# Kernel optimization log

Hardware: AMD Instinct MI355X
Metric: run time of the kernel (lower is better)

Reference implementation:

```python
import jax, jax.numpy as jnp
import numpy as np

IN_FEATURES = 1024
N_CLASSES = 50257
CUTOFFS = [2000, 10000]      # head covers [0,2000); clusters [2000,10000), [10000,50257)
DIV_VALUE = 4.0
IGNORE_INDEX = -1
N_ROWS = 4096
HEAD_SIZE = CUTOFFS[0] + len(CUTOFFS)  # 2002 (head classes + one slot per tail cluster)
HSZ = [int(IN_FEATURES // (DIV_VALUE ** (i + 1))) for i in range(len(CUTOFFS))]  # [256, 64]
BOUNDS = CUTOFFS + [N_CLASSES]


def setup_inputs() -> dict:
    key = jax.random.key(0)
    ks = jax.random.split(key, 8)
    x = jax.random.normal(ks[0], (N_ROWS, IN_FEATURES), dtype=jnp.float32)
    target = jax.random.randint(ks[1], (N_ROWS,), 0, N_CLASSES, dtype=jnp.int64)
    drop = jax.random.uniform(ks[2], (N_ROWS,)) < 0.1
    target = jnp.where(drop, IGNORE_INDEX, target)
    s = 1.0 / np.sqrt(IN_FEATURES)
    head_w = jax.random.normal(ks[3], (HEAD_SIZE, IN_FEATURES), dtype=jnp.float32) * s
    proj0 = jax.random.normal(ks[4], (HSZ[0], IN_FEATURES), dtype=jnp.float32) * s
    out0 = jax.random.normal(ks[5], (BOUNDS[1] - BOUNDS[0], HSZ[0]), dtype=jnp.float32) * (1.0 / np.sqrt(HSZ[0]))
    proj1 = jax.random.normal(ks[6], (HSZ[1], IN_FEATURES), dtype=jnp.float32) * s
    out1 = jax.random.normal(ks[7], (BOUNDS[2] - BOUNDS[1], HSZ[1]), dtype=jnp.float32) * (1.0 / np.sqrt(HSZ[1]))
    return {"x": x, "target": target, "head_w": head_w,
            "proj0": proj0, "out0": out0, "proj1": proj1, "out1": out1}


def reference(x, target, head_w, proj0, out0, proj1, out1):
    # head: [N, cutoff0 + n_clusters] logits, shared log-softmax
    head_lp = jax.nn.log_softmax(jnp.einsum('nd,hd->nh', x, head_w), axis=-1)
    rows = jnp.arange(x.shape[0])
    valid = target != IGNORE_INDEX
    t = jnp.where(valid, target, 0)

    # head-band targets: log prob directly from head
    t_head = jnp.clip(t, 0, CUTOFFS[0] - 1)
    logp = head_lp[rows, t_head]

    # tail clusters: head cluster-slot logprob + within-cluster logprob
    tails = [(proj0, out0), (proj1, out1)]
    for i, (proj, out) in enumerate(tails):
        low, high = BOUNDS[i], BOUNDS[i + 1]
        # [N, hsz] @ [hsz, osz] -> [N, osz] cluster logits
        cl_lp = jax.nn.log_softmax(
            jnp.einsum('nh,oh->no', jnp.einsum('nd,hd->nh', x, proj), out), axis=-1)
        rel = jnp.clip(t - low, 0, high - low - 1)
        cand = head_lp[:, CUTOFFS[0] + i] + cl_lp[rows, rel]
        logp = jnp.where((t >= low) & (t < high), cand, logp)

    # ignore-index filter + mean == masked mean over valid rows
    vf = valid.astype(logp.dtype)
    loss = -(logp * vf).sum() / vf.sum()
    return loss
```

## Files before the change

### kernel.cpp

```cpp
#include <hip/hip_runtime.h>
#include <hip/hip_bf16.h>

typedef __attribute__((ext_vector_type(8))) short bf16x8;
typedef __attribute__((ext_vector_type(4))) float f32x4;
typedef unsigned short u16;

constexpr int NR      = 4096;
constexpr int INF     = 1024;
constexpr int HEAD_N  = 2002;
constexpr int HEAD_NP = 2048;
constexpr int C0_LO   = 2000, C0_HI = 10000;
constexpr int C0_N    = 8000;
constexpr int C1_N    = 40257;
constexpr int C1_NP   = 40320;
constexpr int K0      = 256;
constexpr int K1      = 64;
constexpr int PCAT    = 320;
constexpr int PCAT_P  = 384;
constexpr int WCAT_R  = HEAD_NP + PCAT_P;
constexpr int IGNORE  = -1;
constexpr float LOG2E = 1.4426950408889634f;
constexpr float LN2   = 0.6931471805599453f;

constexpr int S0      = 50;
constexpr int TPS0    = 5;
constexpr int S1      = 40;
constexpr int TPS1    = 8;
constexpr int NHP     = 32;
constexpr int HEADB   = 512;
constexpr int C1B     = 32 * S1;
constexpr int C0B     = 32 * S0;
constexpr int MEGA_GRID = HEADB + C1B + C0B;

static __device__ __forceinline__ u16 f32_to_bf16(float f) {
    unsigned int u = __float_as_uint(f);
    return (u16)((u + 0x7FFFu + ((u >> 16) & 1u)) >> 16);
}
static __device__ __forceinline__ float bf2f(u16 v) {
    unsigned int u = ((unsigned int)v) << 16;
    return __uint_as_float(u);
}

static __device__ __forceinline__ float fast_exp2(float x) {
#if __has_builtin(__builtin_amdgcn_exp2f)
    return __builtin_amdgcn_exp2f(x);
#else
    return __expf(x * LN2);
#endif
}

static __device__ __forceinline__ void gload_lds16(const u16* g, u16* l) {
    __builtin_amdgcn_global_load_lds(
        (const __attribute__((address_space(1))) unsigned int*)g,
        (__attribute__((address_space(3))) unsigned int*)l, 16, 0, 0);
}

struct CvtSegs { const float* s[6]; u16* d[6]; int n8[6]; float sc[6]; };

__global__ void cvt_compact(CvtSegs segs, const int* __restrict__ tgt,
                            int* __restrict__ c0list, int* __restrict__ c1list,
                            int* __restrict__ crow, int* __restrict__ cnts) {
    if (blockIdx.x == 0) {
        __shared__ int b0s, b1s;
        const int tid = threadIdx.x;
        const int lane = tid & 63;
        if (tid == 0) { b0s = 0; b1s = 0; }
        __syncthreads();
        for (int it = 0; it < NR / 256; ++it) {
            const int r = it * 256 + tid;
            const int t = tgt[r];
            const bool in0 = (t >= C0_LO) && (t < C0_HI);
            const bool in1 = (t >= C0_HI);
            unsigned long long m0 = __ballot(in0);
            unsigned long long m1 = __ballot(in1);
            int base0 = 0, base1 = 0;
            if (lane == 0) {
                base0 = atomicAdd(&b0s, (int)__popcll(m0));
                base1 = atomicAdd(&b1s, (int)__popcll(m1));
            }
            base0 = __shfl(base0, 0, 64);
            base1 = __shfl(base1, 0, 64);
            const unsigned long long lt = (1ULL << lane) - 1ULL;
            if (in0) { int s = base0 + (int)__popcll(m0 & lt); c0list[s] = r; crow[r] = s; }
            else if (in1) { int s = base1 + (int)__popcll(m1 & lt); c1list[s] = r; crow[r] = s; }
            else crow[r] = 0;
        }
        __syncthreads();
        const int c0 = b0s, c1 = b1s;
        const int p0 = (c0 + 127) & ~127, p1 = (c1 + 127) & ~127;
        if (threadIdx.x == 0) { cnts[0] = c0; cnts[1] = c1; cnts[2] = p0; cnts[3] = p1; }
        for (int i = c0 + (int)threadIdx.x; i < p0; i += 256) c0list[i] = 0;
        for (int i = c1 + (int)threadIdx.x; i < p1; i += 256) c1list[i] = 0;
    }

    const int stride = gridDim.x * blockDim.x;
    const int gid = blockIdx.x * blockDim.x + threadIdx.x;
#pragma unroll
    for (int seg = 0; seg < 6; ++seg) {
        const float4* sp = (const float4*)segs.s[seg];
        bf16x8* dp = (bf16x8*)segs.d[seg];
        const int n8 = segs.n8[seg];
        const float sc = segs.sc[seg];
        for (int i = gid; i < n8; i += stride) {
            float4 a = sp[2 * i], b = sp[2 * i + 1];
            bf16x8 o;
            o[0] = (short)f32_to_bf16(a.x * sc); o[1] = (short)f32_to_bf16(a.y * sc);
            o[2] = (short)f32_to_bf16(a.z * sc); o[3] = (short)f32_to_bf16(a.w * sc);
            o[4] = (short)f32_to_bf16(b.x * sc); o[5] = (short)f32_to_bf16(b.y * sc);
            o[6] = (short)f32_to_bf16(b.z * sc); o[7] = (short)f32_to_bf16(b.w * sc);
            dp[i] = o;
        }
    }
}

__launch_bounds__(256, 2)
__global__ void proj_tile(const u16* __restrict__ A, const u16* __restrict__ B,
                          u16* __restrict__ HB)
{
    constexpr int K = INF;
    __shared__ u16 ldsA[128 * 64];
    __shared__ u16 ldsB[128 * 64];
    const int tid = threadIdx.x, wid = tid >> 6, lane = tid & 63;
    const int wr = wid >> 1, wc = wid & 1;
    const int row0 = blockIdx.x * 128, col0 = blockIdx.y * 128;

    f32x4 acc[4][4];
#pragma unroll
    for (int m = 0; m < 4; ++m)
#pragma unroll
        for (int n = 0; n < 4; ++n) acc[m][n] = (f32x4){0.f, 0.f, 0.f, 0.f};

    const int srow = lane >> 3;
    const int ssw  = (lane & 7) ^ srow;

    for (int ks = 0; ks < K / 64; ++ks) {
        const int k0 = ks * 64;
#pragma unroll
        for (int q = 0; q < 4; ++q) {
            const int c = q * 4 + wid, row = c * 8 + srow;
            gload_lds16(A + (size_t)(row0 + row) * K + k0 + ssw * 8, ldsA + c * 512);
        }
#pragma unroll
        for (int q = 0; q < 4; ++q) {
            const int c = q * 4 + wid, row = c * 8 + srow;
            gload_lds16(B + (size_t)(col0 + row) * K + k0 + ssw * 8, ldsB + c * 512);
        }
        __syncthreads();
        const bf16x8* A8 = (const bf16x8*)ldsA;
        const bf16x8* B8 = (const bf16x8*)ldsB;
        bf16x8 af[4][2], bfr[4][2];
#pragma unroll
        for (int m = 0; m < 4; ++m) {
            const int ar = wr * 64 + m * 16 + (lane & 15);
#pragma unroll
            for (int ks2 = 0; ks2 < 2; ++ks2)
                af[m][ks2] = A8[ar * 8 + ((ks2 * 4 + (lane >> 4)) ^ (ar & 7))];
        }
#pragma unroll
        for (int n = 0; n < 4; ++n) {
            const int br = wc * 64 + n * 16 + (lane & 15);
#pragma unroll
            for (int ks2 = 0; ks2 < 2; ++ks2)
                bfr[n][ks2] = B8[br * 8 + ((ks2 * 4 + (lane >> 4)) ^ (br & 7))];
        }
#pragma unroll
        for (int ks2 = 0; ks2 < 2; ++ks2)
#pragma unroll
            for (int m = 0; m < 4; ++m)
#pragma unroll
                for (int n = 0; n < 4; ++n)
                    acc[m][n] = __builtin_amdgcn_mfma_f32_16x16x32_bf16(
                        af[m][ks2], bfr[n][ks2], acc[m][n], 0, 0, 0);
        __syncthreads();
    }
#pragma unroll
    for (int m = 0; m < 4; ++m)
#pragma unroll
        for (int n = 0; n < 4; ++n) {
            const int col = col0 + wc * 64 + n * 16 + (lane & 15);
            if (col < PCAT) {
#pragma unroll
                for (int r = 0; r < 4; ++r) {
                    const int row = row0 + wr * 64 + m * 16 + (lane >> 4) * 4 + r;
                    HB[(size_t)row * PCAT + col] = f32_to_bf16(acc[m][n][r]);
                }
            }
        }
}

static __device__ void head_section(int rb, int ct,
                                    const u16* __restrict__ A, const u16* __restrict__ B,
                                    const int* __restrict__ tgt,
                                    float* __restrict__ SEHp, float* __restrict__ TL,
                                    u16* ldsA, u16* ldsB, int* sth)
{
    constexpr int K = INF;
    const int tid = threadIdx.x, wid = tid >> 6, lane = tid & 63;
    const int wr = wid >> 1, wc = wid & 1;
    const int row0 = rb * 128, col0 = ct * 128;

    if (tid < 128) {
        int t = tgt[row0 + tid];
        sth[tid] = (t < 0) ? 0 : (t < C0_LO ? t : (t < C0_HI ? C0_LO : C0_LO + 1));
    }

    f32x4 acc[4][4];
#pragma unroll
    for (int m = 0; m < 4; ++m)
#pragma unroll
        for (int n = 0; n < 4; ++n) acc[m][n] = (f32x4){0.f, 0.f, 0.f, 0.f};

    const int srow = lane >> 3;
    const int ssw  = (lane & 7) ^ srow;

    for (int ks = 0; ks < K / 64; ++ks) {
        const int k0 = ks * 64;
#pragma unroll
        for (int q = 0; q < 4; ++q) {
            const int c = q * 4 + wid, row = c * 8 + srow;
            gload_lds16(A + (size_t)(row0 + row) * K + k0 + ssw * 8, ldsA + c * 512);
        }
#pragma unroll
        for (int q = 0; q < 4; ++q) {
            const int c = q * 4 + wid, row = c * 8 + srow;
            gload_lds16(B + (size_t)(col0 + row) * K + k0 + ssw * 8, ldsB + c * 512);
        }
        __syncthreads();
        const bf16x8* A8 = (const bf16x8*)ldsA;
        const bf16x8* B8 = (const bf16x8*)ldsB;
        bf16x8 af[4][2], bfr[4][2];
#pragma unroll
        for (int m = 0; m < 4; ++m) {
            const int ar = wr * 64 + m * 16 + (lane & 15);
#pragma unroll
            for (int ks2 = 0; ks2 < 2; ++ks2)
                af[m][ks2] = A8[ar * 8 + ((ks2 * 4 + (lane >> 4)) ^ (ar & 7))];
        }
#pragma unroll
        for (int n = 0; n < 4; ++n) {
            const int br = wc * 64 + n * 16 + (lane & 15);
#pragma unroll
            for (int ks2 = 0; ks2 < 2; ++ks2)
                bfr[n][ks2] = B8[br * 8 + ((ks2 * 4 + (lane >> 4)) ^ (br & 7))];
        }
#pragma unroll
        for (int ks2 = 0; ks2 < 2; ++ks2)
#pragma unroll
            for (int m = 0; m < 4; ++m)
#pragma unroll
                for (int n = 0; n < 4; ++n)
                    acc[m][n] = __builtin_amdgcn_mfma_f32_16x16x32_bf16(
                        af[m][ks2], bfr[n][ks2], acc[m][n], 0, 0, 0);
        __syncthreads();
    }

    const int slot = ct * 2 + wc;
#pragma unroll
    for (int m = 0; m < 4; ++m) {
        f32x4 rs = (f32x4){0.f, 0.f, 0.f, 0.f};
#pragma unroll
        for (int n = 0; n < 4; ++n) {
            const int cls = col0 + wc * 64 + n * 16 + (lane & 15);
            if (cls < HEAD_N) {
#pragma unroll
                for (int r = 0; r < 4; ++r) {
                    rs[r] += fast_exp2(acc[m][n][r]);
                    const int lrow = wr * 64 + m * 16 + (lane >> 4) * 4 + r;
                    if (sth[lrow] == cls) TL[row0 + lrow] = acc[m][n][r];
                }
            }
        }
#pragma unroll
        for (int msk = 1; msk < 16; msk <<= 1)
#pragma unroll
            for (int r = 0; r < 4; ++r) rs[r] += __shfl_xor(rs[r], msk, 64);
        if ((lane & 15) == 0) {
            const int rbase = row0 + wr * 64 + m * 16 + (lane >> 4) * 4;
#pragma unroll
            for (int r = 0; r < 4; ++r) SEHp[(size_t)slot * NR + rbase + r] = rs[r];
        }
    }
}

template<int K, int CT>
static __device__ void sumexp_section(const u16* __restrict__ Hbase, int ldh,
                                      const int* __restrict__ list,
                                      const u16* __restrict__ W,
                                      int nreal, int ntiles, int tps,
                                      int rb, int split, float* __restrict__ SEp,
                                      u16* lds)
{
    constexpr int MSETS = 2;
    constexpr int NKF   = K / 32;
    constexpr int SLOTS = K / 8;
    constexpr int CHUNKS = CT * K * 2 / 4096;
    constexpr int RPC   = 256 / SLOTS;
    constexpr int NT    = CT / 16;

    const int tid = threadIdx.x, wid = tid >> 6, lane = tid & 63;
    const int row0 = rb * 128 + wid * 32;

    const int t0 = split * tps;
    const int t1 = min(t0 + tps, ntiles);

    bf16x8 afr[MSETS][NKF];
#pragma unroll
    for (int m = 0; m < MSETS; ++m) {
        const int orow = list[row0 + m * 16 + (lane & 15)];
        const u16* hr = Hbase + (size_t)orow * ldh + (lane >> 4) * 8;
#pragma unroll
        for (int kf = 0; kf < NKF; ++kf)
            afr[m][kf] = *(const bf16x8*)(hr + kf * 32);
    }

    float rs[MSETS][4];
#pragma unroll
    for (int m = 0; m < MSETS; ++m)
#pragma unroll
        for (int r = 0; r < 4; ++r) rs[m][r] = 0.f;

    const int trow  = tid / SLOTS;
    const int swoff = ((tid % SLOTS) ^ (trow & 7)) * 8;

    auto STAGE = [&](int t, int buf) {
        const u16* wb = W + (size_t)t * CT * K + (size_t)trow * K + swoff;
        u16* lb = lds + buf * (CT * K) + wid * 512;
#pragma unroll
        for (int c = 0; c < CHUNKS; ++c)
            gload_lds16(wb + (size_t)c * RPC * K, lb + c * 2048);
    };

    int cur = 0;
    STAGE(t0, 0);
    __syncthreads();

    for (int t = t0; t < t1; ++t) {
        if (t + 1 < t1) STAGE(t + 1, cur ^ 1);
        const bf16x8* B8 = (const bf16x8*)(lds + cur * (CT * K));
        const bool full = (t + 1) * CT <= nreal;
#pragma unroll
        for (int n = 0; n < NT; ++n) {
            const int br = n * 16 + (lane & 15);
            bf16x8 bfr[NKF];
#pragma unroll
            for (int kf = 0; kf < NKF; ++kf)
                bfr[kf] = B8[br * SLOTS + ((kf * 4 + (lane >> 4)) ^ (br & 7))];
            f32x4 acc[MSETS];
#pragma unroll
            for (int m = 0; m < MSETS; ++m) acc[m] = (f32x4){0.f, 0.f, 0.f, 0.f};
#pragma unroll
            for (int m = 0; m < MSETS; ++m)
#pragma unroll
                for (int kf = 0; kf < NKF; ++kf)
                    acc[m] = __builtin_amdgcn_mfma_f32_16x16x32_bf16(
                        afr[m][kf], bfr[kf], acc[m], 0, 0, 0);
            if (full || (t * CT + n * 16 + (lane & 15)) < nreal) {
#pragma unroll
                for (int m = 0; m < MSETS; ++m)
#pragma unroll
                    for (int r = 0; r < 4; ++r) rs[m][r] += fast_exp2(acc[m][r]);
            }
        }
        __syncthreads();
        cur ^= 1;
    }

#pragma unroll
    for (int msk = 1; msk < 16; msk <<= 1)
#pragma unroll
        for (int m = 0; m < MSETS; ++m)
#pragma unroll
            for (int r = 0; r < 4; ++r) rs[m][r] += __shfl_xor(rs[m][r], msk, 64);
    if ((lane & 15) == 0) {
        const int rbase = row0 + (lane >> 4) * 4;
#pragma unroll
        for (int m = 0; m < MSETS; ++m)
#pragma unroll
            for (int r = 0; r < 4; ++r)
                SEp[(size_t)split * NR + rbase + m * 16 + r] = rs[m][r];
    }
}

__launch_bounds__(256, 4)
__global__ void mega_kernel(const u16* __restrict__ xb, const u16* __restrict__ wcatb,
                            const u16* __restrict__ hcatb,
                            const u16* __restrict__ o0b, const u16* __restrict__ o1b,
                            const int* __restrict__ tgt,
                            const int* __restrict__ c0list, const int* __restrict__ c1list,
                            const int* __restrict__ cnts,
                            float* __restrict__ SEHp, float* __restrict__ TL,
                            float* __restrict__ C0p, float* __restrict__ C1p)
{
    __shared__ u16 smem[2][8192];
    __shared__ int sth[128];
    const int bid = blockIdx.x;

    if (bid < HEADB) {
        head_section(bid >> 4, bid & 15, xb, wcatb, tgt, SEHp, TL,
                     smem[0], smem[1], sth);
    } else if (bid < HEADB + C1B) {
        const int c = bid - HEADB;
        const int rb = c / S1, split = c - rb * S1;
        if (rb * 128 < cnts[3])
            sumexp_section<K1, 128>(hcatb + 256, PCAT, c1list, o1b,
                                    C1_N, C1_NP / 128, TPS1, rb, split, C1p, smem[0]);
    } else {
        const int idx = bid - (HEADB + C1B);
        const int rb = idx / S0, split = idx - rb * S0;
        if (rb * 128 < cnts[2])
            sumexp_section<K0, 32>(hcatb, PCAT, c0list, o0b,
                                   C0_N, C0_N / 32, TPS0, rb, split, C0p, smem[0]);
    }
}

__global__ void epilogue_kernel(const int* __restrict__ tgt, const float* __restrict__ tl,
                                const float* __restrict__ out0, const float* __restrict__ out1,
                                const u16* __restrict__ hcatb,
                                const float* __restrict__ SEHp, const float* __restrict__ C0p,
                                const float* __restrict__ C1p, const int* __restrict__ crow,
                                float* __restrict__ rowlogp, float* __restrict__ rowvalid) {
    const int wid = threadIdx.x >> 6, lane = threadIdx.x & 63;
    const int r = blockIdx.x * 4 + wid;
    const int t = tgt[r];
    const bool valid = (t != IGNORE);
    const int tc = valid ? t : 0;
    const int band = (tc < C0_LO) ? 0 : (tc < C0_HI) ? 1 : 2;
    const int cr = crow[r];

    float p2 = 0.f;
    if (band == 1) {
        const u16* hr = hcatb + (size_t)r * PCAT;
        const float* crp = out0 + (size_t)(tc - C0_LO) * K0;
        for (int k = lane; k < K0; k += 64) p2 += bf2f(hr[k]) * crp[k];
    } else if (band == 2) {
        p2 = bf2f(hcatb[(size_t)r * PCAT + 256 + lane]) * out1[(size_t)(tc - C0_HI) * K1 + lane];
    }
#pragma unroll
    for (int msk = 32; msk >= 1; msk >>= 1) p2 += __shfl_xor(p2, msk, 64);

    float hp = (lane < NHP) ? SEHp[(size_t)lane * NR + r] : 0.f;
    float cp = 0.f;
    if (band == 1 && lane < S0) cp = C0p[(size_t)lane * NR + cr];
    if (band == 2 && lane < S1) cp = C1p[(size_t)lane * NR + cr];
#pragma unroll
    for (int msk = 1; msk < 64; msk <<= 1) {
        hp += __shfl_xor(hp, msk, 64);
        cp += __shfl_xor(cp, msk, 64);
    }

    if (lane == 0) {
        float logp = LN2 * tl[r] - __logf(hp);
        if (band != 0) logp += p2 - __logf(cp);
        rowlogp[r]  = valid ? logp : 0.f;
        rowvalid[r] = valid ? 1.f : 0.f;
    }
}

__global__ void final_reduce(const float* __restrict__ rowlogp,
                             const float* __restrict__ rowvalid, float* __restrict__ out) {
    __shared__ float sl[256], sv[256];
    const int tid = threadIdx.x;
    float a = 0.f, b = 0.f;
    for (int i = tid; i < NR; i += 256) { a += rowlogp[i]; b += rowvalid[i]; }
    sl[tid] = a; sv[tid] = b;
    __syncthreads();
    for (int s = 128; s > 0; s >>= 1) {
        if (tid < s) { sl[tid] += sl[tid + s]; sv[tid] += sv[tid + s]; }
        __syncthreads();
    }
    if (tid == 0) out[0] = -sl[0] / sv[0];
}

extern "C" void kernel_launch(void* const* d_in, const int* in_sizes, int n_in,
                              void* d_out, int out_size, void* d_ws, size_t ws_size,
                              hipStream_t stream) {
    const float* x      = (const float*)d_in[0];
    const int*   tgt    = (const int*)d_in[1];
    const float* head_w = (const float*)d_in[2];
    const float* proj0  = (const float*)d_in[3];
    const float* out0   = (const float*)d_in[4];
    const float* proj1  = (const float*)d_in[5];
    const float* out1   = (const float*)d_in[6];
    float* loss = (float*)d_out;

    char* base = (char*)d_ws;
    size_t off = 0;
    auto alloc = [&](size_t bytes) { char* p = base + off; off += (bytes + 255) & ~(size_t)255; return p; };

    u16* xb    = (u16*)alloc((size_t)NR * INF * 2);
    u16* wcatb = (u16*)alloc((size_t)WCAT_R * INF * 2);
    u16* o0b   = (u16*)alloc((size_t)C0_N * K0 * 2);
    u16* o1b   = (u16*)alloc((size_t)C1_NP * K1 * 2);
    u16* hcatb = (u16*)alloc((size_t)NR * PCAT * 2);
    float* SEHp = (float*)alloc((size_t)NHP * NR * 4);
    float* C0p  = (float*)alloc((size_t)S0 * NR * 4);
    float* C1p  = (float*)alloc((size_t)S1 * NR * 4);
    float* tl   = (float*)alloc((size_t)NR * 4);
    int* c0list = (int*)alloc((size_t)(NR + 128) * 4);
    int* c1list = (int*)alloc((size_t)(NR + 128) * 4);
    int* crow   = (int*)alloc((size_t)NR * 4);
    int* cnts   = (int*)alloc(4 * 4);
    float* rowlogp  = (float*)alloc((size_t)NR * 4);
    float* rowvalid = (float*)alloc((size_t)NR * 4);

    CvtSegs segs;
    segs.s[0] = x;      segs.d[0] = xb;                              segs.n8[0] = NR * INF / 8;      segs.sc[0] = 1.0f;
    segs.s[1] = head_w; segs.d[1] = wcatb;                           segs.n8[1] = HEAD_N * INF / 8;  segs.sc[1] = LOG2E;
    segs.s[2] = proj0;  segs.d[2] = wcatb + (size_t)HEAD_NP * INF;   segs.n8[2] = 256 * INF / 8;     segs.sc[2] = 1.0f;
    segs.s[3] = proj1;  segs.d[3] = wcatb + (size_t)(HEAD_NP + 256) * INF; segs.n8[3] = 64 * INF / 8; segs.sc[3] = 1.0f;
    segs.s[4] = out0;   segs.d[4] = o0b;                             segs.n8[4] = C0_N * K0 / 8;     segs.sc[4] = LOG2E;
    segs.s[5] = out1;   segs.d[5] = o1b;                             segs.n8[5] = C1_N * K1 / 8;     segs.sc[5] = LOG2E;
    cvt_compact<<<2048, 256, 0, stream>>>(segs, tgt, c0list, c1list, crow, cnts);

    proj_tile<<<dim3(32, PCAT_P / 128), 256, 0, stream>>>(xb, wcatb + (size_t)HEAD_NP * INF, hcatb);

    mega_kernel<<<MEGA_GRID, 256, 0, stream>>>(xb, wcatb, hcatb, o0b, o1b, tgt,
                                               c0list, c1list, cnts, SEHp, tl, C0p, C1p);

    epilogue_kernel<<<NR / 4, 256, 0, stream>>>(tgt, tl, out0, out1, hcatb,
                                                SEHp, C0p, C1p, crow, rowlogp, rowvalid);
    final_reduce<<<1, 256, 0, stream>>>(rowlogp, rowvalid, loss);
    (void)in_sizes; (void)n_in; (void)out_size; (void)ws_size;
}
```

Before: 88.86 us.

## Fuse projection GEMM into conversion kernel and interleave mega-kernel work with grid-stride loops

Removes the separate proj_tile launch by computing the x·[proj0;proj1] projection inside the conversion kernel. Dedicated blocks read fp32 x and proj weights directly, convert them to bf16 in registers and run MFMA without LDS staging, while the remaining blocks convert x, head_w, out0 and out1. The mega-kernel now interleaves head, cluster-1 and cluster-0 work across block IDs and uses grid-stride loops bounded by the actual compacted counts, so fewer blocks exit idle. In exchange, the fused projection reloads proj rows from global memory per warp without tiling reuse, which may be slow and sits on the critical path of the conversion kernel.

```diff
diff --git a/kernel.cpp b/kernel.cpp
--- a/kernel.cpp
+++ b/kernel.cpp
@@ -16,8 +16,6 @@
 constexpr int K0      = 256;
 constexpr int K1      = 64;
 constexpr int PCAT    = 320;
-constexpr int PCAT_P  = 384;
-constexpr int WCAT_R  = HEAD_NP + PCAT_P;
 constexpr int IGNORE  = -1;
 constexpr float LOG2E = 1.4426950408889634f;
 constexpr float LN2   = 0.6931471805599453f;
@@ -27,10 +25,9 @@
 constexpr int S1      = 40;
 constexpr int TPS1    = 8;
 constexpr int NHP     = 32;
-constexpr int HEADB   = 512;
-constexpr int C1B     = 32 * S1;
-constexpr int C0B     = 32 * S0;
-constexpr int MEGA_GRID = HEADB + C1B + C0B;
+constexpr int NPROJB  = 128;
+constexpr int CVT_GRID = 2048;
+constexpr int MEGA_GRID = 1792;
 
 static __device__ __forceinline__ u16 f32_to_bf16(float f) {
     unsigned int u = __float_as_uint(f);
@@ -39,6 +36,14 @@
 static __device__ __forceinline__ float bf2f(u16 v) {
     unsigned int u = ((unsigned int)v) << 16;
     return __uint_as_float(u);
+}
+static __device__ __forceinline__ bf16x8 cvt8(float4 a, float4 b, float sc) {
+    bf16x8 o;
+    o[0] = (short)f32_to_bf16(a.x * sc); o[1] = (short)f32_to_bf16(a.y * sc);
+    o[2] = (short)f32_to_bf16(a.z * sc); o[3] = (short)f32_to_bf16(a.w * sc);
+    o[4] = (short)f32_to_bf16(b.x * sc); o[5] = (short)f32_to_bf16(b.y * sc);
+    o[6] = (short)f32_to_bf16(b.z * sc); o[7] = (short)f32_to_bf16(b.w * sc);
+    return o;
 }
 
 static __device__ __forceinline__ float fast_exp2(float x) {
@@ -55,15 +60,53 @@
         (__attribute__((address_space(3))) unsigned int*)l, 16, 0, 0);
 }
 
-struct CvtSegs { const float* s[6]; u16* d[6]; int n8[6]; float sc[6]; };
-
-__global__ void cvt_compact(CvtSegs segs, const int* __restrict__ tgt,
-                            int* __restrict__ c0list, int* __restrict__ c1list,
-                            int* __restrict__ crow, int* __restrict__ cnts) {
-    if (blockIdx.x == 0) {
+struct CvtSegs { const float* s[4]; u16* d[4]; int n8[4]; float sc[4]; };
+
+__global__ void cvtproj_kernel(CvtSegs segs,
+                               const float* __restrict__ x,
+                               const float* __restrict__ proj0, const float* __restrict__ proj1,
+                               u16* __restrict__ hcatb,
+                               const int* __restrict__ tgt,
+                               int* __restrict__ c0list, int* __restrict__ c1list,
+                               int* __restrict__ crow, int* __restrict__ cnts) {
+    const int bid = blockIdx.x;
+    const int tid = threadIdx.x;
+    const int wid = tid >> 6, lane = tid & 63;
+
+    if (bid < NPROJB) {
+        const int gw = bid * 4 + wid;
+        const int rg = gw >> 1;
+        const int cs = gw & 1;
+        const int row = rg * 16 + (lane & 15);
+        const int koff = (lane >> 4) * 8;
+        f32x4 acc[10];
+#pragma unroll
+        for (int n = 0; n < 10; ++n) acc[n] = (f32x4){0.f, 0.f, 0.f, 0.f};
+        for (int kf = 0; kf < 32; ++kf) {
+            const float* xr = x + (size_t)row * INF + kf * 32 + koff;
+            bf16x8 av = cvt8(*(const float4*)xr, *(const float4*)(xr + 4), 1.0f);
+#pragma unroll
+            for (int n = 0; n < 10; ++n) {
+                const int p = cs * 160 + n * 16 + (lane & 15);
+                const float* pr = (p < 256 ? proj0 + (size_t)p * INF
+                                           : proj1 + (size_t)(p - 256) * INF) + kf * 32 + koff;
+                bf16x8 bv = cvt8(*(const float4*)pr, *(const float4*)(pr + 4), 1.0f);
+                acc[n] = __builtin_amdgcn_mfma_f32_16x16x32_bf16(av, bv, acc[n], 0, 0, 0);
+            }
+        }
+        const int orow = rg * 16 + (lane >> 4) * 4;
+#pragma unroll
+        for (int n = 0; n < 10; ++n) {
+            const int col = cs * 160 + n * 16 + (lane & 15);
+#pragma unroll
+            for (int r = 0; r < 4; ++r)
+                hcatb[(size_t)(orow + r) * PCAT + col] = f32_to_bf16(acc[n][r]);
+        }
+        return;
+    }
+
+    if (bid == NPROJB) {
         __shared__ int b0s, b1s;
-        const int tid = threadIdx.x;
-        const int lane = tid & 63;
         if (tid == 0) { b0s = 0; b1s = 0; }
         __syncthreads();
         for (int it = 0; it < NR / 256; ++it) {
@@ -88,104 +131,23 @@
         __syncthreads();
         const int c0 = b0s, c1 = b1s;
         const int p0 = (c0 + 127) & ~127, p1 = (c1 + 127) & ~127;
-        if (threadIdx.x == 0) { cnts[0] = c0; cnts[1] = c1; cnts[2] = p0; cnts[3] = p1; }
-        for (int i = c0 + (int)threadIdx.x; i < p0; i += 256) c0list[i] = 0;
-        for (int i = c1 + (int)threadIdx.x; i < p1; i += 256) c1list[i] = 0;
-    }
-
-    const int stride = gridDim.x * blockDim.x;
-    const int gid = blockIdx.x * blockDim.x + threadIdx.x;
-#pragma unroll
-    for (int seg = 0; seg < 6; ++seg) {
+        if (tid == 0) { cnts[0] = c0; cnts[1] = c1; cnts[2] = p0; cnts[3] = p1; }
+        for (int i = c0 + tid; i < p0; i += 256) c0list[i] = 0;
+        for (int i = c1 + tid; i < p1; i += 256) c1list[i] = 0;
+    }
+
+    const int cid = bid - NPROJB;
+    const int stride = (CVT_GRID - NPROJB) * 256;
+    const int gid = cid * 256 + tid;
+#pragma unroll
+    for (int seg = 0; seg < 4; ++seg) {
         const float4* sp = (const float4*)segs.s[seg];
         bf16x8* dp = (bf16x8*)segs.d[seg];
         const int n8 = segs.n8[seg];
         const float sc = segs.sc[seg];
-        for (int i = gid; i < n8; i += stride) {
-            float4 a = sp[2 * i], b = sp[2 * i + 1];
-            bf16x8 o;
-            o[0] = (short)f32_to_bf16(a.x * sc); o[1] = (short)f32_to_bf16(a.y * sc);
-            o[2] = (short)f32_to_bf16(a.z * sc); o[3] = (short)f32_to_bf16(a.w * sc);
-            o[4] = (short)f32_to_bf16(b.x * sc); o[5] = (short)f32_to_bf16(b.y * sc);
-            o[6] = (short)f32_to_bf16(b.z * sc); o[7] = (short)f32_to_bf16(b.w * sc);
-            dp[i] = o;
-        }
-    }
-}
-
-__launch_bounds__(256, 2)
-__global__ void proj_tile(const u16* __restrict__ A, const u16* __restrict__ B,
-                          u16* __restrict__ HB)
-{
-    constexpr int K = INF;
-    __shared__ u16 ldsA[128 * 64];
-    __shared__ u16 ldsB[128 * 64];
-    const int tid = threadIdx.x, wid = tid >> 6, lane = tid & 63;
-    const int wr = wid >> 1, wc = wid & 1;
-    const int row0 = blockIdx.x * 128, col0 = blockIdx.y * 128;
-
-    f32x4 acc[4][4];
-#pragma unroll
-    for (int m = 0; m < 4; ++m)
-#pragma unroll
-        for (int n = 0; n < 4; ++n) acc[m][n] = (f32x4){0.f, 0.f, 0.f, 0.f};
-
-    const int srow = lane >> 3;
-    const int ssw  = (lane & 7) ^ srow;
-
-    for (int ks = 0; ks < K / 64; ++ks) {
-        const int k0 = ks * 64;
-#pragma unroll
-        for (int q = 0; q < 4; ++q) {
-            const int c = q * 4 + wid, row = c * 8 + srow;
-            gload_lds16(A + (size_t)(row0 + row) * K + k0 + ssw * 8, ldsA + c * 512);
-        }
-#pragma unroll
-        for (int q = 0; q < 4; ++q) {
-            const int c = q * 4 + wid, row = c * 8 + srow;
-            gload_lds16(B + (size_t)(col0 + row) * K + k0 + ssw * 8, ldsB + c * 512);
-        }
-        __syncthreads();
-        const bf16x8* A8 = (const bf16x8*)ldsA;
-        const bf16x8* B8 = (const bf16x8*)ldsB;
-        bf16x8 af[4][2], bfr[4][2];
-#pragma unroll
-        for (int m = 0; m < 4; ++m) {
-            const int ar = wr * 64 + m * 16 + (lane & 15);
-#pragma unroll
-            for (int ks2 = 0; ks2 < 2; ++ks2)
-                af[m][ks2] = A8[ar * 8 + ((ks2 * 4 + (lane >> 4)) ^ (ar & 7))];
-        }
-#pragma unroll
-        for (int n = 0; n < 4; ++n) {
-            const int br = wc * 64 + n * 16 + (lane & 15);
-#pragma unroll
-            for (int ks2 = 0; ks2 < 2; ++ks2)
-                bfr[n][ks2] = B8[br * 8 + ((ks2 * 4 + (lane >> 4)) ^ (br & 7))];
-        }
-#pragma unroll
-        for (int ks2 = 0; ks2 < 2; ++ks2)
-#pragma unroll
-            for (int m = 0; m < 4; ++m)
-#pragma unroll
-                for (int n = 0; n < 4; ++n)
-                    acc[m][n] = __builtin_amdgcn_mfma_f32_16x16x32_bf16(
-                        af[m][ks2], bfr[n][ks2], acc[m][n], 0, 0, 0);
-        __syncthreads();
-    }
-#pragma unroll
-    for (int m = 0; m < 4; ++m)
-#pragma unroll
-        for (int n = 0; n < 4; ++n) {
-            const int col = col0 + wc * 64 + n * 16 + (lane & 15);
-            if (col < PCAT) {
-#pragma unroll
-                for (int r = 0; r < 4; ++r) {
-                    const int row = row0 + wr * 64 + m * 16 + (lane >> 4) * 4 + r;
-                    HB[(size_t)row * PCAT + col] = f32_to_bf16(acc[m][n][r]);
-                }
-            }
-        }
+        for (int i = gid; i < n8; i += stride)
+            dp[i] = cvt8(sp[2 * i], sp[2 * i + 1], sc);
+    }
 }
 
 static __device__ void head_section(int rb, int ct,
@@ -382,7 +344,7 @@
 }
 
 __launch_bounds__(256, 4)
-__global__ void mega_kernel(const u16* __restrict__ xb, const u16* __restrict__ wcatb,
+__global__ void mega_kernel(const u16* __restrict__ xb, const u16* __restrict__ whb,
                             const u16* __restrict__ hcatb,
                             const u16* __restrict__ o0b, const u16* __restrict__ o1b,
                             const int* __restrict__ tgt,
@@ -394,22 +356,24 @@
     __shared__ u16 smem[2][8192];
     __shared__ int sth[128];
     const int bid = blockIdx.x;
-
-    if (bid < HEADB) {
-        head_section(bid >> 4, bid & 15, xb, wcatb, tgt, SEHp, TL,
+    const int q = bid / 7, g = bid % 7;
+
+    if (g < 2) {
+        const int h = q * 2 + g;
+        head_section(h >> 4, h & 15, xb, whb, tgt, SEHp, TL,
                      smem[0], smem[1], sth);
-    } else if (bid < HEADB + C1B) {
-        const int c = bid - HEADB;
-        const int rb = c / S1, split = c - rb * S1;
-        if (rb * 128 < cnts[3])
+    } else if (g < 6) {
+        const int c = q * 4 + (g - 2);
+        const int W1 = (cnts[3] >> 7) * S1;
+        for (int w = c; w < W1; w += 1024)
             sumexp_section<K1, 128>(hcatb + 256, PCAT, c1list, o1b,
-                                    C1_N, C1_NP / 128, TPS1, rb, split, C1p, smem[0]);
+                                    C1_N, C1_NP / 128, TPS1, w / S1, w % S1, C1p, smem[0]);
     } else {
-        const int idx = bid - (HEADB + C1B);
-        const int rb = idx / S0, split = idx - rb * S0;
-        if (rb * 128 < cnts[2])
+        const int c = q;
+        const int W0 = (cnts[2] >> 7) * S0;
+        for (int w = c; w < W0; w += 256)
             sumexp_section<K0, 32>(hcatb, PCAT, c0list, o0b,
-                                   C0_N, C0_N / 32, TPS0, rb, split, C0p, smem[0]);
+                                   C0_N, C0_N / 32, TPS0, w / S0, w % S0, C0p, smem[0]);
     }
 }
 
@@ -488,7 +452,7 @@
     auto alloc = [&](size_t bytes) { char* p = base + off; off += (bytes + 255) & ~(size_t)255; return p; };
 
     u16* xb    = (u16*)alloc((size_t)NR * INF * 2);
-    u16* wcatb = (u16*)alloc((size_t)WCAT_R * INF * 2);
+    u16* whb   = (u16*)alloc((size_t)HEAD_NP * INF * 2);
     u16* o0b   = (u16*)alloc((size_t)C0_N * K0 * 2);
     u16* o1b   = (u16*)alloc((size_t)C1_NP * K1 * 2);
     u16* hcatb = (u16*)alloc((size_t)NR * PCAT * 2);
@@ -504,17 +468,14 @@
     float* rowvalid = (float*)alloc((size_t)NR * 4);
 
     CvtSegs segs;
-    segs.s[0] = x;      segs.d[0] = xb;                              segs.n8[0] = NR * INF / 8;      segs.sc[0] = 1.0f;
-    segs.s[1] = head_w; segs.d[1] = wcatb;                           segs.n8[1] = HEAD_N * INF / 8;  segs.sc[1] = LOG2E;
-    segs.s[2] = proj0;  segs.d[2] = wcatb + (size_t)HEAD_NP * INF;   segs.n8[2] = 256 * INF / 8;     segs.sc[2] = 1.0f;
-    segs.s[3] = proj1;  segs.d[3] = wcatb + (size_t)(HEAD_NP + 256) * INF; segs.n8[3] = 64 * INF / 8; segs.sc[3] = 1.0f;
-    segs.s[4] = out0;   segs.d[4] = o0b;                             segs.n8[4] = C0_N * K0 / 8;     segs.sc[4] = LOG2E;
-    segs.s[5] = out1;   segs.d[5] = o1b;                             segs.n8[5] = C1_N * K1 / 8;     segs.sc[5] = LOG2E;
-    cvt_compact<<<2048, 256, 0, stream>>>(segs, tgt, c0list, c1list, crow, cnts);
-
-    proj_tile<<<dim3(32, PCAT_P / 128), 256, 0, stream>>>(xb, wcatb + (size_t)HEAD_NP * INF, hcatb);
-
-    mega_kernel<<<MEGA_GRID, 256, 0, stream>>>(xb, wcatb, hcatb, o0b, o1b, tgt,
+    segs.s[0] = x;      segs.d[0] = xb;   segs.n8[0] = NR * INF / 8;      segs.sc[0] = 1.0f;
+    segs.s[1] = head_w; segs.d[1] = whb;  segs.n8[1] = HEAD_N * INF / 8;  segs.sc[1] = LOG2E;
+    segs.s[2] = out0;   segs.d[2] = o0b;  segs.n8[2] = C0_N * K0 / 8;     segs.sc[2] = LOG2E;
+    segs.s[3] = out1;   segs.d[3] = o1b;  segs.n8[3] = C1_N * K1 / 8;     segs.sc[3] = LOG2E;
+    cvtproj_kernel<<<CVT_GRID, 256, 0, stream>>>(segs, x, proj0, proj1, hcatb,
+                                                 tgt, c0list, c1list, crow, cnts);
+
+    mega_kernel<<<MEGA_GRID, 256, 0, stream>>>(xb, whb, hcatb, o0b, o1b, tgt,
                                                c0list, c1list, cnts, SEHp, tl, C0p, C1p);
 
     epilogue_kernel<<<NR / 4, 256, 0, stream>>>(tgt, tl, out0, out1, hcatb,
```

Measured after the change: 201.9 us. +127.3%, slower.

## Interleave head and cluster work in a persistent fixed-size mega-kernel grid

Applied to the files above, without the earlier changes.

Shrinks the mega-kernel grid to a fixed block count and interleaves roles across blocks in a 7-slot pattern: 2 head, 4 cluster-1 and 1 cluster-0. Cluster blocks loop over a work list sized from the actual row counts, so no blocks are launched only to exit early, and the heavy tail work is mixed in with head work instead of queued after it. The risk is load imbalance: cluster-0 work gets only a quarter of the cluster-1 slots and has to loop many times per block. The work count now uses a floor division by 128, which could drop a partial row block if the counts are not padded.

```diff
diff --git a/kernel.cpp b/kernel.cpp
--- a/kernel.cpp
+++ b/kernel.cpp
@@ -27,10 +27,7 @@
 constexpr int S1      = 40;
 constexpr int TPS1    = 8;
 constexpr int NHP     = 32;
-constexpr int HEADB   = 512;
-constexpr int C1B     = 32 * S1;
-constexpr int C0B     = 32 * S0;
-constexpr int MEGA_GRID = HEADB + C1B + C0B;
+constexpr int MEGA_GRID = 1792;
 
 static __device__ __forceinline__ u16 f32_to_bf16(float f) {
     unsigned int u = __float_as_uint(f);
@@ -382,7 +379,7 @@
 }
 
 __launch_bounds__(256, 4)
-__global__ void mega_kernel(const u16* __restrict__ xb, const u16* __restrict__ wcatb,
+__global__ void mega_kernel(const u16* __restrict__ xb, const u16* __restrict__ whb,
                             const u16* __restrict__ hcatb,
                             const u16* __restrict__ o0b, const u16* __restrict__ o1b,
                             const int* __restrict__ tgt,
@@ -394,22 +391,24 @@
     __shared__ u16 smem[2][8192];
     __shared__ int sth[128];
     const int bid = blockIdx.x;
-
-    if (bid < HEADB) {
-        head_section(bid >> 4, bid & 15, xb, wcatb, tgt, SEHp, TL,
+    const int q = bid / 7, g = bid % 7;
+
+    if (g < 2) {
+        const int h = q * 2 + g;
+        head_section(h >> 4, h & 15, xb, whb, tgt, SEHp, TL,
                      smem[0], smem[1], sth);
-    } else if (bid < HEADB + C1B) {
-        const int c = bid - HEADB;
-        const int rb = c / S1, split = c - rb * S1;
-        if (rb * 128 < cnts[3])
+    } else if (g < 6) {
+        const int c = q * 4 + (g - 2);
+        const int W1 = (cnts[3] >> 7) * S1;
+        for (int w = c; w < W1; w += 1024)
             sumexp_section<K1, 128>(hcatb + 256, PCAT, c1list, o1b,
-                                    C1_N, C1_NP / 128, TPS1, rb, split, C1p, smem[0]);
+                                    C1_N, C1_NP / 128, TPS1, w / S1, w % S1, C1p, smem[0]);
     } else {
-        const int idx = bid - (HEADB + C1B);
-        const int rb = idx / S0, split = idx - rb * S0;
-        if (rb * 128 < cnts[2])
+        const int c = q;
+        const int W0 = (cnts[2] >> 7) * S0;
+        for (int w = c; w < W0; w += 256)
             sumexp_section<K0, 32>(hcatb, PCAT, c0list, o0b,
-                                   C0_N, C0_N / 32, TPS0, rb, split, C0p, smem[0]);
+                                   C0_N, C0_N / 32, TPS0, w / S0, w % S0, C0p, smem[0]);
     }
 }
 
```

Measured after the change: 98.85 us. 1.11x slower.
